# Kernel optimization log

Measured on AMD Instinct MI355X. Metric: run time of the kernel, lower is better.

The kernel has to match this reference:

```python
import jax, jax.numpy as jnp
import numpy as np
from jax import lax

WIN = 7            # win_size
K = 0.03           # stability constant
COV_NORM = WIN * WIN / (WIN * WIN - 1.0)  # faithful: win_size**2 / (win_size**2 - 1)


def setup_inputs() -> dict:
    key = jax.random.key(0)
    kx, ky = jax.random.split(key)
    x = jax.random.normal(kx, (2, 4, 160, 160, 96), dtype=jnp.float32)
    y = jax.random.randint(ky, (2, 1, 160, 160, 96), 0, 4, dtype=jnp.int64)
    return {"x": x, "y": y}


def _box_mean(a):
    s = lax.reduce_window(a, jnp.array(0, a.dtype), lax.add,
                          (1, 1, WIN, WIN, WIN), (1, 1, 1, 1, 1), 'VALID')
    return s / jnp.asarray(WIN ** 3, a.dtype)


def reference(x, y):
    B, C, H, W, D = x.shape
    # one_hot(y, num_classes=C): (B,1,H,W,D) int -> (B,C,H,W,D) float
    y1 = jnp.moveaxis(jax.nn.one_hot(y[:, 0], C, dtype=x.dtype), -1, 1)
    xr = x.reshape(-1, 1, H, W, D)
    yr = y1.reshape(-1, 1, H, W, D)
    xr = xr * yr
    data_range = jnp.max(yr)
    xr = jax.nn.sigmoid(xr)
    c = (K * data_range) ** 2 / 2
    ux = _box_mean(xr)
    uy = _box_mean(yr)
    uxx = _box_mean(xr * xr)
    uyy = _box_mean(yr * yr)
    uxy = _box_mean(xr * yr)
    vx = COV_NORM * (uxx - ux * ux)
    vy = COV_NORM * (uyy - uy * uy)
    vxy = COV_NORM * (uxy - ux * uy)
    s_value = (vxy + c) / (vx * vy + c)
    return 1.0 - jnp.mean(s_value)
```

## Files before the change

### kernel.cpp

```cpp
#include <hip/hip_runtime.h>
#include <hip/hip_fp16.h>

#define WINS 7
#define H 160
#define W 160
#define DD 96
#define HO 154
#define WO 154
#define DOUT 90
#define CSTRIDE (H*W*DD)

#define TH 8
#define TW 8
#define TD 16
#define IH 14
#define IW 14
#define NCOL (IH * IW)
#define IDU 22
#define NDP 11
#define ID 24
#define NV 6
#define NITEMS (NCOL * NV)
#define HTILES 20
#define WTILES 20
#define DTILES 6
#define DPB2 24

struct alignas(8) Half4 { __half x, y, z, w; };

static __device__ __forceinline__ __half2 u2h(unsigned int a) {
    __half2 r; __builtin_memcpy(&r, &a, 4); return r;
}
static __device__ __forceinline__ unsigned int h2u(__half2 v) {
    unsigned int r; __builtin_memcpy(&r, &v, 4); return r;
}
static __device__ __forceinline__ void pmask(__half2 v, __half2& p, __half2& m) {
    const unsigned int bits = h2u(v);
    const unsigned int neg  = bits & 0x80008000u;
    const unsigned int full = (neg >> 15) * 0xFFFFu;
    p = u2h(bits & ~full);
    m = u2h(((~bits >> 15) & 0x00010001u) * 0x3C00u);
}

__device__ __forceinline__ float sval(float c0, float c1, float c2) {
    const float S_t  = c1 + 0.5f  * (343.0f - c0);
    const float S_t2 = c2 + 0.25f * (343.0f - c0);
    const float inv  = 1.0f / 343.0f;
    const float ux   = S_t  * inv;
    const float uy   = c0   * inv;
    const float uxx  = S_t2 * inv;
    const float uxy  = c1   * inv;
    const float covn = 49.0f / 48.0f;
    const float cc   = 0.00045f;
    const float vx  = covn * (uxx - ux * ux);
    const float vy  = covn * (uy  - uy * uy);
    const float vxy = covn * (uxy - ux * uy);
    return (vxy + cc) * __builtin_amdgcn_rcpf(vx * vy + cc);
}

__global__ __launch_bounds__(256)
void sigmoid_prepass(const float* __restrict__ x,
                     const int* __restrict__ y,
                     __half* __restrict__ xs) {
    const int b  = blockIdx.y;
    const int qv = blockIdx.x * 256 + threadIdx.x;
    const int off = 4 * qv;
    const int4 yv = *(const int4*)(y + (size_t)b * CSTRIDE + off);
#pragma unroll
    for (int c = 0; c < 4; c++) {
        const size_t xo = ((size_t)(b * 4 + c)) * CSTRIDE + off;
        const float4 xv = *(const float4*)(x + xo);
        const float s0 = 1.0f / (1.0f + __expf(-xv.x));
        const float s1 = 1.0f / (1.0f + __expf(-xv.y));
        const float s2 = 1.0f / (1.0f + __expf(-xv.z));
        const float s3 = 1.0f / (1.0f + __expf(-xv.w));
        Half4 hv;
        hv.x = __float2half((yv.x == c) ? s0 : -s0);
        hv.y = __float2half((yv.y == c) ? s1 : -s1);
        hv.z = __float2half((yv.z == c) ? s2 : -s2);
        hv.w = __float2half((yv.w == c) ? s3 : -s3);
        *(Half4*)(xs + xo) = hv;
    }
}

template <bool PRE>
__global__ __launch_bounds__(256, 5)
void structure_loss_main(const float* __restrict__ x,
                         const int* __restrict__ y,
                         const __half* __restrict__ xs,
                         double* __restrict__ acc) {
    __shared__ __half sA0[IH * TW * IDU];
    __shared__ __half sA1[IH * TW * IDU];
    __shared__ __half sA2[IH * TW * IDU];
    __shared__ union alignas(16) {
        __half vs[NCOL * ID];
        struct {
            __half b0[TH * TW * DPB2];
            __half b1[TH * TW * DPB2];
            __half b2[TH * TW * DPB2];
        } sb;
    } u;
    __shared__ unsigned int yb[NCOL * 2];
    __shared__ float wsum[4];

    const int dt = blockIdx.x;
    const int wt = blockIdx.y;
    const int z  = blockIdx.z;
    const int b  = z / HTILES;
    const int ht = z - b * HTILES;

    const int h0 = ht * TH, w0 = wt * TW, d0 = dt * TD;
    const int* yc = y + (size_t)b * (size_t)CSTRIDE;
    const int t = threadIdx.x;

    if (!PRE) {
        for (int i = t; i < NCOL * 2; i += 256) {
            const int col = i >> 1, hf = i & 1;
            const int ih = col / IW, iw = col - ih * IW;
            const int h = min(h0 + ih, H - 1);
            const int w = min(w0 + iw, W - 1);
            const size_t cb = (size_t)(h * W + w) * DD;
            const int dstart = d0 + 12 * hf;
            unsigned int pk = 0u;
#pragma unroll
            for (int j3 = 0; j3 < 3; j3++) {
                const int dbase = dstart + 4 * j3;
                if (dbase < DD) {
                    const int4 yv = *(const int4*)(yc + cb + dbase);
                    pk |= (unsigned)(yv.x & 3) << (2 * (4 * j3 + 0));
                    pk |= (unsigned)(yv.y & 3) << (2 * (4 * j3 + 1));
                    pk |= (unsigned)(yv.z & 3) << (2 * (4 * j3 + 2));
                    pk |= (unsigned)(yv.w & 3) << (2 * (4 * j3 + 3));
                }
            }
            yb[i] = pk;
        }
        __syncthreads();
    }

    float lsum = 0.f;

    for (int cl = 0; cl < 4; cl++) {
        if (PRE) {
            const __half* xsc = xs + ((size_t)b * 4 + cl) * (size_t)CSTRIDE;
#pragma unroll
            for (int k = 0; k < 3; k++) {
                const int i = t + 256 * k;
                if (i < NCOL * 3) {
                    const int col = i / 3, q = i - col * 3;
                    const int ih = col / IW, iw = col - ih * IW;
                    const int h = min(h0 + ih, H - 1);
                    const int w = min(w0 + iw, W - 1);
                    const int dbase = d0 + 8 * q;
                    uint4 vv = make_uint4(0u, 0u, 0u, 0u);
                    if (dbase < DD)
                        vv = *(const uint4*)(xsc + (h * W + w) * DD + dbase);
                    *(uint4*)&u.vs[col * ID + 8 * q] = vv;
                }
            }
        } else {
            const float* xc = x + ((size_t)b * 4 + cl) * (size_t)CSTRIDE;
#pragma unroll
            for (int k = 0; k < 5; k++) {
                const int i = t + 256 * k;
                if (i < NITEMS) {
                    const int col = i / NV, q = i - col * NV;
                    const int ih = col / IW, iw = col - ih * IW;
                    const int h = min(h0 + ih, H - 1);
                    const int w = min(w0 + iw, W - 1);
                    const int dbase = d0 + 4 * q;
                    Half4 hv;
                    hv.x = hv.y = hv.z = hv.w = __float2half(0.f);
                    if (dbase < DD) {
                        const float4 xv = *(const float4*)(xc + (h * W + w) * DD + dbase);
                        const int wsel = (q >= 3) ? 1 : 0;
                        const unsigned int pk =
                            yb[col * 2 + wsel] >> (8 * (q - 3 * wsel));
                        const float s0 = 1.0f / (1.0f + __expf(-xv.x));
                        const float s1 = 1.0f / (1.0f + __expf(-xv.y));
                        const float s2 = 1.0f / (1.0f + __expf(-xv.z));
                        const float s3 = 1.0f / (1.0f + __expf(-xv.w));
                        hv.x = __float2half(((int)((pk >> 0) & 3u) == cl) ? s0 : -s0);
                        hv.y = __float2half(((int)((pk >> 2) & 3u) == cl) ? s1 : -s1);
                        hv.z = __float2half(((int)((pk >> 4) & 3u) == cl) ? s2 : -s2);
                        hv.w = __float2half(((int)((pk >> 6) & 3u) == cl) ? s3 : -s3);
                    }
                    *(Half4*)&u.vs[col * ID + 4 * q] = hv;
                }
            }
        }
        __syncthreads();

        if (t < IH * NDP) {
            const int ih = t / NDP, dp = t - ih * NDP;
            const int dd = 2 * dp;
            const __half2 z2 = __float2half2_rn(0.f);
            __half2 v2[IW];
            const int vbase = ih * IW * ID + dd;
#pragma unroll
            for (int iw = 0; iw < IW; iw++)
                v2[iw] = *(const __half2*)&u.vs[vbase + iw * ID];
            __half2 sm = z2, sp = z2, sq = z2;
#pragma unroll
            for (int iw = 0; iw < WINS; iw++) {
                __half2 p, m;
                pmask(v2[iw], p, m);
                sm = __hadd2(sm, m);
                sp = __hadd2(sp, p);
                sq = __hfma2(p, v2[iw], sq);
            }
            int o = (ih * TW) * IDU + dd;
            *(__half2*)&sA0[o] = sm;
            *(__half2*)&sA1[o] = sp;
            *(__half2*)&sA2[o] = sq;
#pragma unroll
            for (int wo = 1; wo < TW; wo++) {
                const __half2 a = v2[wo + 6], bb = v2[wo - 1];
                __half2 pa, ma, pb, mb;
                pmask(a, pa, ma);
                pmask(bb, pb, mb);
                sm = __hadd2(sm, __hsub2(ma, mb));
                sp = __hadd2(sp, __hsub2(pa, pb));
                sq = __hadd2(sq, __hsub2(__hmul2(pa, a), __hmul2(pb, bb)));
                o += IDU;
                *(__half2*)&sA0[o] = sm;
                *(__half2*)&sA1[o] = sp;
                *(__half2*)&sA2[o] = sq;
            }
        }
        __syncthreads();

        if (t < 2 * TW * NDP) {
            const int dp = t % NDP;
            const int r  = t / NDP;
            const int wo = r & 7;
            const int ho0 = (r >> 3) * 4;
            const int dd = 2 * dp;
            __half2 a0[10], a1[10], a2[10];
#pragma unroll
            for (int k = 0; k < 10; k++) {
                const int idx = ((ho0 + k) * TW + wo) * IDU + dd;
                a0[k] = *(const __half2*)&sA0[idx];
                a1[k] = *(const __half2*)&sA1[idx];
                a2[k] = *(const __half2*)&sA2[idx];
            }
            __half2 s0 = a0[0], s1 = a1[0], s2 = a2[0];
#pragma unroll
            for (int k = 1; k < WINS; k++) {
                s0 = __hadd2(s0, a0[k]);
                s1 = __hadd2(s1, a1[k]);
                s2 = __hadd2(s2, a2[k]);
            }
            int o = (ho0 * TW + wo) * DPB2 + dd;
            *(__half2*)&u.sb.b0[o] = s0;
            *(__half2*)&u.sb.b1[o] = s1;
            *(__half2*)&u.sb.b2[o] = s2;
#pragma unroll
            for (int k = 1; k < 4; k++) {
                s0 = __hadd2(s0, __hsub2(a0[k + 6], a0[k - 1]));
                s1 = __hadd2(s1, __hsub2(a1[k + 6], a1[k - 1]));
                s2 = __hadd2(s2, __hsub2(a2[k + 6], a2[k - 1]));
                o += TW * DPB2;
                *(__half2*)&u.sb.b0[o] = s0;
                *(__half2*)&u.sb.b1[o] = s1;
                *(__half2*)&u.sb.b2[o] = s2;
            }
        }
        __syncthreads();

        {
            const int dq = t & 3;
            const int wo = (t >> 2) & 7;
            const int ho = t >> 5;
            const int hg = h0 + ho, wg = w0 + wo;
            if (hg < HO && wg < WO) {
                const int base = (ho * TW + wo) * DPB2 + dq * 4;
                float b0[10], b1[10], b2[10];
#pragma unroll
                for (int k = 0; k < 5; k++) {
                    float2 f;
                    f = __half22float2(*(const __half2*)&u.sb.b0[base + 2 * k]);
                    b0[2 * k] = f.x; b0[2 * k + 1] = f.y;
                    f = __half22float2(*(const __half2*)&u.sb.b1[base + 2 * k]);
                    b1[2 * k] = f.x; b1[2 * k + 1] = f.y;
                    f = __half22float2(*(const __half2*)&u.sb.b2[base + 2 * k]);
                    b2[2 * k] = f.x; b2[2 * k + 1] = f.y;
                }
                float s0 = 0.f, s1 = 0.f, s2 = 0.f;
#pragma unroll
                for (int k = 0; k < WINS; k++) { s0 += b0[k]; s1 += b1[k]; s2 += b2[k]; }
                const int dg = d0 + dq * 4;
#pragma unroll
                for (int k = 0; k < 4; k++) {
                    if (k > 0) {
                        s0 += b0[k + 6] - b0[k - 1];
                        s1 += b1[k + 6] - b1[k - 1];
                        s2 += b2[k + 6] - b2[k - 1];
                    }
                    if (dg + k < DOUT) lsum += sval(s0, s1, s2);
                }
            }
        }
        __syncthreads();
    }

#pragma unroll
    for (int off = 32; off > 0; off >>= 1) lsum += __shfl_down(lsum, off, 64);
    const int wave = t >> 6;
    if ((t & 63) == 0) wsum[wave] = lsum;
    __syncthreads();
    if (t == 0) {
        const float s = wsum[0] + wsum[1] + wsum[2] + wsum[3];
        atomicAdd(acc, (double)s);
    }
}

__global__ void structure_loss_finalize(const double* __restrict__ acc,
                                        float* __restrict__ out) {
    out[0] = 1.0f - (float)(acc[0] / 17075520.0);
}

extern "C" void kernel_launch(void* const* d_in, const int* in_sizes, int n_in,
                              void* d_out, int out_size, void* d_ws, size_t ws_size,
                              hipStream_t stream) {
    const float* x = (const float*)d_in[0];
    const int*   y = (const int*)d_in[1];
    double* acc = (double*)d_ws;
    __half* xs = (__half*)((char*)d_ws + 16);

    (void)hipMemsetAsync(d_ws, 0, sizeof(double), stream);

    const size_t need = 16 + (size_t)8 * CSTRIDE * sizeof(__half);
    dim3 grid(DTILES, WTILES, 2 * HTILES);

    if (ws_size >= need) {
        sigmoid_prepass<<<dim3(2400, 2), 256, 0, stream>>>(x, y, xs);
        structure_loss_main<true><<<grid, 256, 0, stream>>>(x, y, xs, acc);
    } else {
        structure_loss_main<false><<<grid, 256, 0, stream>>>(x, y, xs, acc);
    }
    structure_loss_finalize<<<1, 1, 0, stream>>>(acc, (float*)d_out);
}
```

Before: 209.6 us.

## Use direct global-to-LDS loads, interleave LDS partial sums, fuse finalize via last-block

Tile loads of the half-precision prepass buffer now use global_load_lds to go straight to shared memory, with clamped addresses instead of zero-fill. The three per-stage shared arrays are interleaved into one padded __half2 layout to change bank access patterns. The memset and the finalize kernel are removed: the prepass zeroes the accumulator and a ticket counter, and the last main block writes the output. Clamping the depth index past the end loads real data instead of zeros into padded lanes, which relies on those lanes being masked later.

Measured after the change: 324.6 us. 1.55x slower.

```diff
diff --git a/kernel.cpp b/kernel.cpp
--- a/kernel.cpp
+++ b/kernel.cpp
@@ -16,7 +16,6 @@
 #define IH 14
 #define IW 14
 #define NCOL (IH * IW)
-#define IDU 22
 #define NDP 11
 #define ID 24
 #define NV 6
@@ -24,9 +23,15 @@
 #define HTILES 20
 #define WTILES 20
 #define DTILES 6
-#define DPB2 24
+#define NBLK (DTILES * WTILES * 2 * HTILES)
+
+#define RSA 293
+#define SBP 13
 
 struct alignas(8) Half4 { __half x, y, z, w; };
+
+typedef const __attribute__((address_space(1))) unsigned int glds_g;
+typedef __attribute__((address_space(3))) unsigned int glds_l;
 
 static __device__ __forceinline__ __half2 u2h(unsigned int a) {
     __half2 r; __builtin_memcpy(&r, &a, 4); return r;
@@ -61,7 +66,12 @@
 __global__ __launch_bounds__(256)
 void sigmoid_prepass(const float* __restrict__ x,
                      const int* __restrict__ y,
-                     __half* __restrict__ xs) {
+                     __half* __restrict__ xs,
+                     double* __restrict__ acc) {
+    if (blockIdx.x == 0 && blockIdx.y == 0 && threadIdx.x == 0) {
+        acc[0] = 0.0;
+        ((unsigned long long*)acc)[1] = 0ull;
+    }
     const int b  = blockIdx.y;
     const int qv = blockIdx.x * 256 + threadIdx.x;
     const int off = 4 * qv;
@@ -88,17 +98,12 @@
 void structure_loss_main(const float* __restrict__ x,
                          const int* __restrict__ y,
                          const __half* __restrict__ xs,
-                         double* __restrict__ acc) {
-    __shared__ __half sA0[IH * TW * IDU];
-    __shared__ __half sA1[IH * TW * IDU];
-    __shared__ __half sA2[IH * TW * IDU];
+                         double* __restrict__ acc,
+                         float* __restrict__ out) {
+    __shared__ __half2 sA2[IH * RSA];
     __shared__ union alignas(16) {
-        __half vs[NCOL * ID];
-        struct {
-            __half b0[TH * TW * DPB2];
-            __half b1[TH * TW * DPB2];
-            __half b2[TH * TW * DPB2];
-        } sb;
+        __half  vs[NCOL * ID];
+        __half2 sb2[TH * TW * SBP * 3];
     } u;
     __shared__ unsigned int yb[NCOL * 2];
     __shared__ float wsum[4];
@@ -151,11 +156,12 @@
                     const int ih = col / IW, iw = col - ih * IW;
                     const int h = min(h0 + ih, H - 1);
                     const int w = min(w0 + iw, W - 1);
-                    const int dbase = d0 + 8 * q;
-                    uint4 vv = make_uint4(0u, 0u, 0u, 0u);
-                    if (dbase < DD)
-                        vv = *(const uint4*)(xsc + (h * W + w) * DD + dbase);
-                    *(uint4*)&u.vs[col * ID + 8 * q] = vv;
+                    const int dbase = min(d0 + 8 * q, DD - 8);
+                    const __half* gp = xsc + (size_t)((h * W + w) * DD + dbase);
+                    __half* lp = &u.vs[col * ID + 8 * q];
+                    __builtin_amdgcn_global_load_lds((glds_g*)(const void*)gp,
+                                                     (glds_l*)(void*)lp,
+                                                     16, 0, 0);
                 }
             }
         } else {
@@ -209,10 +215,8 @@
                 sp = __hadd2(sp, p);
                 sq = __hfma2(p, v2[iw], sq);
             }
-            int o = (ih * TW) * IDU + dd;
-            *(__half2*)&sA0[o] = sm;
-            *(__half2*)&sA1[o] = sp;
-            *(__half2*)&sA2[o] = sq;
+            int o = ih * RSA + dp * 3;
+            sA2[o] = sm; sA2[o + 1] = sp; sA2[o + 2] = sq;
 #pragma unroll
             for (int wo = 1; wo < TW; wo++) {
                 const __half2 a = v2[wo + 6], bb = v2[wo - 1];
@@ -222,10 +226,8 @@
                 sm = __hadd2(sm, __hsub2(ma, mb));
                 sp = __hadd2(sp, __hsub2(pa, pb));
                 sq = __hadd2(sq, __hsub2(__hmul2(pa, a), __hmul2(pb, bb)));
-                o += IDU;
-                *(__half2*)&sA0[o] = sm;
-                *(__half2*)&sA1[o] = sp;
-                *(__half2*)&sA2[o] = sq;
+                o += NDP * 3;
+                sA2[o] = sm; sA2[o + 1] = sp; sA2[o + 2] = sq;
             }
         }
         __syncthreads();
@@ -235,14 +237,13 @@
             const int r  = t / NDP;
             const int wo = r & 7;
             const int ho0 = (r >> 3) * 4;
-            const int dd = 2 * dp;
             __half2 a0[10], a1[10], a2[10];
 #pragma unroll
             for (int k = 0; k < 10; k++) {
-                const int idx = ((ho0 + k) * TW + wo) * IDU + dd;
-                a0[k] = *(const __half2*)&sA0[idx];
-                a1[k] = *(const __half2*)&sA1[idx];
-                a2[k] = *(const __half2*)&sA2[idx];
+                const int idx = (ho0 + k) * RSA + (wo * NDP + dp) * 3;
+                a0[k] = sA2[idx];
+                a1[k] = sA2[idx + 1];
+                a2[k] = sA2[idx + 2];
             }
             __half2 s0 = a0[0], s1 = a1[0], s2 = a2[0];
 #pragma unroll
@@ -251,19 +252,15 @@
                 s1 = __hadd2(s1, a1[k]);
                 s2 = __hadd2(s2, a2[k]);
             }
-            int o = (ho0 * TW + wo) * DPB2 + dd;
-            *(__half2*)&u.sb.b0[o] = s0;
-            *(__half2*)&u.sb.b1[o] = s1;
-            *(__half2*)&u.sb.b2[o] = s2;
+            int o = ((ho0 * TW + wo) * SBP + dp) * 3;
+            u.sb2[o] = s0; u.sb2[o + 1] = s1; u.sb2[o + 2] = s2;
 #pragma unroll
             for (int k = 1; k < 4; k++) {
                 s0 = __hadd2(s0, __hsub2(a0[k + 6], a0[k - 1]));
                 s1 = __hadd2(s1, __hsub2(a1[k + 6], a1[k - 1]));
                 s2 = __hadd2(s2, __hsub2(a2[k + 6], a2[k - 1]));
-                o += TW * DPB2;
-                *(__half2*)&u.sb.b0[o] = s0;
-                *(__half2*)&u.sb.b1[o] = s1;
-                *(__half2*)&u.sb.b2[o] = s2;
+                o += TW * SBP * 3;
+                u.sb2[o] = s0; u.sb2[o + 1] = s1; u.sb2[o + 2] = s2;
             }
         }
         __syncthreads();
@@ -274,16 +271,17 @@
             const int ho = t >> 5;
             const int hg = h0 + ho, wg = w0 + wo;
             if (hg < HO && wg < WO) {
-                const int base = (ho * TW + wo) * DPB2 + dq * 4;
+                const int colb = (ho * TW + wo) * SBP;
                 float b0[10], b1[10], b2[10];
 #pragma unroll
                 for (int k = 0; k < 5; k++) {
+                    const int rd = (colb + 2 * dq + k) * 3;
                     float2 f;
-                    f = __half22float2(*(const __half2*)&u.sb.b0[base + 2 * k]);
+                    f = __half22float2(u.sb2[rd + 0]);
                     b0[2 * k] = f.x; b0[2 * k + 1] = f.y;
-                    f = __half22float2(*(const __half2*)&u.sb.b1[base + 2 * k]);
+                    f = __half22float2(u.sb2[rd + 1]);
                     b1[2 * k] = f.x; b1[2 * k + 1] = f.y;
-                    f = __half22float2(*(const __half2*)&u.sb.b2[base + 2 * k]);
+                    f = __half22float2(u.sb2[rd + 2]);
                     b2[2 * k] = f.x; b2[2 * k + 1] = f.y;
                 }
                 float s0 = 0.f, s1 = 0.f, s2 = 0.f;
@@ -310,14 +308,16 @@
     if ((t & 63) == 0) wsum[wave] = lsum;
     __syncthreads();
     if (t == 0) {
-        const float s = wsum[0] + wsum[1] + wsum[2] + wsum[3];
-        atomicAdd(acc, (double)s);
-    }
-}
-
-__global__ void structure_loss_finalize(const double* __restrict__ acc,
-                                        float* __restrict__ out) {
-    out[0] = 1.0f - (float)(acc[0] / 17075520.0);
+        const double s = (double)(wsum[0] + wsum[1] + wsum[2] + wsum[3]);
+        atomicAdd(acc, s);
+        __threadfence();
+        unsigned long long* tk = (unsigned long long*)(acc + 1);
+        if (atomicAdd(tk, 1ull) == (unsigned long long)(NBLK - 1)) {
+            __threadfence();
+            const double tot = atomicAdd(acc, 0.0);
+            out[0] = 1.0f - (float)(tot / 17075520.0);
+        }
+    }
 }
 
 extern "C" void kernel_launch(void* const* d_in, const int* in_sizes, int n_in,
@@ -328,16 +328,16 @@
     double* acc = (double*)d_ws;
     __half* xs = (__half*)((char*)d_ws + 16);
 
-    (void)hipMemsetAsync(d_ws, 0, sizeof(double), stream);
-
     const size_t need = 16 + (size_t)8 * CSTRIDE * sizeof(__half);
     dim3 grid(DTILES, WTILES, 2 * HTILES);
 
     if (ws_size >= need) {
-        sigmoid_prepass<<<dim3(2400, 2), 256, 0, stream>>>(x, y, xs);
-        structure_loss_main<true><<<grid, 256, 0, stream>>>(x, y, xs, acc);
+        sigmoid_prepass<<<dim3(2400, 2), 256, 0, stream>>>(x, y, xs, acc);
+        structure_loss_main<true><<<grid, 256, 0, stream>>>(x, y, xs, acc,
+                                                            (float*)d_out);
     } else {
-        structure_loss_main<false><<<grid, 256, 0, stream>>>(x, y, xs, acc);
-    }
-    structure_loss_finalize<<<1, 1, 0, stream>>>(acc, (float*)d_out);
-}
+        (void)hipMemsetAsync(d_ws, 0, 16, stream);
+        structure_loss_main<false><<<grid, 256, 0, stream>>>(x, y, xs, acc,
+                                                             (float*)d_out);
+    }
+}
```
